# Optimization experiments

Hardware: AMD Instinct MI355X
Metric: run time of the kernel (lower is better)

Reference implementation:

```python
import math
import jax, jax.numpy as jnp
import numpy as np

B, S, HIDDEN = 1, 4096, 2048
HEADS, KVH = 16, 4
HD = HIDDEN // HEADS            # 128
GROUPS = HEADS // KVH           # 4
CHUNK = 1024                    # ring_attention_chunk_size
BASE = 500000.0
MAXPOS = 131072
ORIG = 8192
BFAST, BSLOW, MSCALE_CFG = 32.0, 1.0, 1.0
SCALING = MAXPOS / ORIG


def _yarn_inv_freq():
    dim = HD
    pos_freqs = BASE ** (np.arange(0, dim, 2, dtype=np.float32) / dim)
    extrap = 1.0 / pos_freqs
    interp = 1.0 / (SCALING * pos_freqs)
    low = max(math.floor(dim * math.log(ORIG / (BFAST * 2 * math.pi)) / (2 * math.log(BASE))), 0)
    high = min(math.ceil(dim * math.log(ORIG / (BSLOW * 2 * math.pi)) / (2 * math.log(BASE))), dim - 1)
    i = np.arange(dim // 2, dtype=np.float32)
    smooth = np.clip((i - low) / max(high - low, 1), 0.0, 1.0)  # i<low -> interp, i>high -> extrap
    inv = (1.0 - smooth) * interp + smooth * extrap
    return jnp.asarray(inv, jnp.float32)

INV_FREQ = _yarn_inv_freq()
MSCALE = (0.1 * math.log(SCALING) + 1.0) * MSCALE_CFG  # scaling > 1


def rotate_half(x):
    x1, x2 = jnp.split(x, 2, axis=-1)
    return jnp.concatenate((-x2, x1), axis=-1)


def ring_attention(q, k, v, chunk, causal=True):
    # q,k,v: [B,H,S,D]; kv_len divisible by chunk
    b, h, s, d = q.shape
    kv_len = k.shape[2]
    nc = kv_len // chunk
    scale = d ** (-0.5)
    k_chunks = jnp.moveaxis(k.reshape(b, h, nc, chunk, d), 2, 0)  # [nc,B,H,chunk,D]
    v_chunks = jnp.moveaxis(v.reshape(b, h, nc, chunk, d), 2, 0)
    kv_starts = jnp.arange(nc) * chunk
    q_idx = jnp.arange(s)[:, None]
    k_off = jnp.arange(chunk)[None, :]
    neg_inf = jnp.float32(-jnp.inf)

    def step(carry, inp):
        out, mx, se = carry
        kch, vch, kv_start = inp
        scores = jnp.einsum('bhqd,bhkd->bhqk', q, kch) * scale
        if causal:
            mask = (kv_start + k_off) > q_idx  # [S, chunk]
            scores = jnp.where(mask[None, None], neg_inf, scores)
        chunk_max = scores.max(axis=-1, keepdims=True)
        new_max = jnp.maximum(mx, chunk_max)
        exp_old = se * jnp.exp(mx - new_max)
        exp_chunk = jnp.exp(scores - new_max)
        exp_sum_chunk = exp_chunk.sum(axis=-1, keepdims=True)
        denom = exp_old + exp_sum_chunk + 1e-10
        out = out * (se / denom) + jnp.einsum('bhqk,bhkd->bhqd', exp_chunk, vch) / denom
        return (out, new_max, exp_old + exp_sum_chunk), None

    init = (jnp.zeros_like(q),
            jnp.full((b, h, s, 1), -jnp.inf, dtype=q.dtype),
            jnp.zeros((b, h, s, 1), dtype=q.dtype))
    (out, _, _), _ = jax.lax.scan(step, init, (k_chunks, v_chunks, kv_starts))
    return out


def setup_inputs() -> dict:
    key = jax.random.key(0)
    ks = jax.random.split(key, 5)
    hidden_states = jax.random.normal(ks[0], (B, S, HIDDEN), dtype=jnp.float32)
    position_ids = jnp.broadcast_to(jnp.arange(S, dtype=jnp.int32)[None, :], (B, S))
    sd = 1.0 / math.sqrt(HIDDEN)
    Wq = jax.random.normal(ks[1], (HIDDEN, HEADS * HD), dtype=jnp.float32) * sd
    Wk = jax.random.normal(ks[2], (HIDDEN, KVH * HD), dtype=jnp.float32) * sd
    Wv = jax.random.normal(ks[3], (HIDDEN, KVH * HD), dtype=jnp.float32) * sd
    Wo = jax.random.normal(ks[4], (HEADS * HD, HIDDEN), dtype=jnp.float32) * sd
    return {'hidden_states': hidden_states, 'position_ids': position_ids,
            'Wq': Wq, 'Wk': Wk, 'Wv': Wv, 'Wo': Wo}


def reference(hidden_states, position_ids, Wq, Wk, Wv, Wo):
    b, s, _ = hidden_states.shape
    q = (hidden_states @ Wq).reshape(b, s, HEADS, HD).transpose(0, 2, 1, 3)
    k = (hidden_states @ Wk).reshape(b, s, KVH, HD).transpose(0, 2, 1, 3)
    v = (hidden_states @ Wv).reshape(b, s, KVH, HD).transpose(0, 2, 1, 3)
    # YaRN rope
    freqs = position_ids.astype(jnp.float32)[:, :, None] * INV_FREQ[None, None, :]  # [B,S,HD/2]
    emb = jnp.concatenate((freqs, freqs), axis=-1)  # [B,S,HD]
    cos = (jnp.cos(emb) * MSCALE)[:, None]  # [B,1,S,HD]
    sin = (jnp.sin(emb) * MSCALE)[:, None]
    q = q * cos + rotate_half(q) * sin
    k = k * cos + rotate_half(k) * sin
    # GQA expand
    k = jnp.repeat(k, GROUPS, axis=1)
    v = jnp.repeat(v, GROUPS, axis=1)
    # ring path: use_ring_attention and kv_len > chunk
    attn = ring_attention(q, k, v, CHUNK, causal=True)
    attn = attn.transpose(0, 2, 1, 3).reshape(b, s, HEADS * HD)
    return attn @ Wo
```

## Files before the change

kernel.cpp:

```cpp
#include <hip/hip_runtime.h>
#include <cstdint>
#include <cstddef>


typedef unsigned short u16;
typedef unsigned int u32;
typedef float f32x4 __attribute__((ext_vector_type(4)));
typedef __bf16 bf16x8 __attribute__((ext_vector_type(8)));

__device__ __forceinline__ u16 f2bf(float f) {
    union { float f; u32 u; } v; v.f = f;
    u32 u = v.u;
    u += 0x7fffu + ((u >> 16) & 1u);
    return (u16)(u >> 16);
}
__device__ __forceinline__ float bf2f(u16 b) {
    union { u32 u; float f; } v; v.u = ((u32)b) << 16;
    return v.f;
}
__device__ __forceinline__ u16 f2h(float f) {
    union { _Float16 h; u16 u; } v; v.h = (_Float16)f; return v.u;
}
__device__ __forceinline__ float h2f(u16 u) {
    union { u16 u; _Float16 h; } v; v.u = u; return (float)v.h;
}

__device__ __forceinline__ void load16_to_lds(const void* g, void* l) {
    __builtin_amdgcn_global_load_lds((const __attribute__((address_space(1))) u32*)g,
                                     (__attribute__((address_space(3))) u32*)l,
                                     16, 0, 0);
}

#define MFMA16(a, b, c) __builtin_amdgcn_mfma_f32_16x16x32_bf16((a), (b), (c), 0, 0, 0)

__global__ __launch_bounds__(256) void convert_f32_bf16(const float* __restrict__ X,
                                                        u16* __restrict__ Y) {
    const int base = (blockIdx.x * 1024 + threadIdx.x) * 4;
#pragma unroll
    for (int k = 0; k < 4; ++k) {
        const int i = base + k * 1024;
        const float4 v = *(const float4*)(X + i);
        union { u16 s[4]; uint2 u; } pk;
        pk.s[0] = f2bf(v.x); pk.s[1] = f2bf(v.y); pk.s[2] = f2bf(v.z); pk.s[3] = f2bf(v.w);
        *(uint2*)(Y + i) = pk.u;
    }
}

__global__ __launch_bounds__(256) void transpose_w4(const float* __restrict__ Wq,
                                                    const float* __restrict__ Wk,
                                                    const float* __restrict__ Wv,
                                                    const float* __restrict__ Wo,
                                                    u16* __restrict__ Wt,
                                                    u16* __restrict__ Wot) {
    __shared__ float tile[64][65];
    const int bx = blockIdx.x;
    const float* W; u16* dst; int N, n0;
    if (bx < 32)      { W = Wq; dst = Wt;                          N = 2048; n0 = bx * 64; }
    else if (bx < 40) { W = Wk; dst = Wt + (size_t)2048 * 2048;    N = 512;  n0 = (bx - 32) * 64; }
    else if (bx < 48) { W = Wv; dst = Wt + (size_t)2560 * 2048;    N = 512;  n0 = (bx - 40) * 64; }
    else              { W = Wo; dst = Wot;                         N = 2048; n0 = (bx - 48) * 64; }
    const int k0 = blockIdx.y * 64;
    const int tc = threadIdx.x & 63, tr = threadIdx.x >> 6;
#pragma unroll
    for (int i = 0; i < 64; i += 4)
        tile[tc][tr + i] = W[(size_t)(k0 + tr + i) * N + n0 + tc];
    __syncthreads();
#pragma unroll
    for (int i = 0; i < 64; i += 4)
        dst[(size_t)(n0 + tr + i) * 2048 + k0 + tc] = f2bf(tile[tr + i][tc]);
}

__device__ __forceinline__ void store_out(float* p, float v) { *p = v; }
__device__ __forceinline__ void store_out(u16* p, float v) { *p = f2bf(v); }

template <typename OutT>
__global__ __launch_bounds__(256) void gemm_bt(const u16* __restrict__ A,
                                               const u16* __restrict__ Bt,
                                               OutT* __restrict__ C,
                                               int M, int N, int K) {
    __shared__ __align__(16) u16 sA[8192];
    __shared__ __align__(16) u16 sB[8192];
    const int t = threadIdx.x;
    const int lane = t & 63, w = t >> 6;
    const int quad = lane >> 4, l15 = lane & 15;
    const int m0 = blockIdx.x << 7, n0 = blockIdx.y << 7;
    const int wr4 = (w >> 1) * 4, wc4 = (w & 1) * 4;
    f32x4 acc[4][4] = {};
    for (int k0 = 0; k0 < K; k0 += 64) {
        __syncthreads();
#pragma unroll
        for (int r = 0; r < 2; ++r) {
            const int f = w * 2 + r;
#pragma unroll
            for (int kc = 0; kc < 2; ++kc) {
                load16_to_lds(A + (size_t)(m0 + f * 16 + l15) * K + k0 + kc * 32 + quad * 8,
                              sA + (f * 2 + kc) * 512);
                load16_to_lds(Bt + (size_t)(n0 + f * 16 + l15) * K + k0 + kc * 32 + quad * 8,
                              sB + (f * 2 + kc) * 512);
            }
        }
        __syncthreads();
#pragma unroll
        for (int kc = 0; kc < 2; ++kc) {
            bf16x8 af[4], bb[4];
#pragma unroll
            for (int i = 0; i < 4; ++i)
                af[i] = *(const bf16x8*)(sA + ((wr4 + i) * 2 + kc) * 512 + lane * 8);
#pragma unroll
            for (int j = 0; j < 4; ++j)
                bb[j] = *(const bf16x8*)(sB + ((wc4 + j) * 2 + kc) * 512 + lane * 8);
#pragma unroll
            for (int i = 0; i < 4; ++i)
#pragma unroll
                for (int j = 0; j < 4; ++j)
                    acc[i][j] = MFMA16(af[i], bb[j], acc[i][j]);
        }
    }
#pragma unroll
    for (int i = 0; i < 4; ++i)
#pragma unroll
        for (int j = 0; j < 4; ++j) {
            const int row = m0 + (w >> 1) * 64 + i * 16 + quad * 4;
            const int col = n0 + (w & 1) * 64 + j * 16 + l15;
#pragma unroll
            for (int r = 0; r < 4; ++r)
                store_out(C + (size_t)(row + r) * N + col, acc[i][j][r]);
        }
}

__global__ __launch_bounds__(256) void rope_vt_kernel(u16* __restrict__ QKV,
                                                      u16* __restrict__ Vt,
                                                      const int* __restrict__ pos_ids) {
    __shared__ u16 tile[64 * 72];
    if (blockIdx.x >= 20480) {
        const int b = blockIdx.x - 20480;
        const int k0 = (b & 63) * 64, d0 = ((b >> 6) & 1) * 64, kvh = b >> 7;
        const int t = threadIdx.x;
#pragma unroll
        for (int k = 0; k < 4; ++k) {
            const int u = t + k * 256;
            const int key = u >> 4, dg = u & 15;
            const uint2 v = *(const uint2*)(QKV + (size_t)(k0 + key) * 3072 + 2560 + kvh * 128 + d0 + dg * 4);
            *(uint2*)(tile + key * 72 + dg * 4) = v;
        }
        __syncthreads();
#pragma unroll
        for (int k = 0; k < 4; ++k) {
            const int u = t + k * 256;
            const int d = u >> 4, kg = u & 15;
            union { u16 s[4]; uint2 v; } pk;
#pragma unroll
            for (int i = 0; i < 4; ++i) pk.s[i] = tile[(kg * 4 + i) * 72 + d];
            *(uint2*)(Vt + (size_t)(kvh * 128 + d0 + d) * 4096 + k0 + kg * 4) = pk.v;
        }
        return;
    }
    const int idx = blockIdx.x * 256 + threadIdx.x;
    const int NQ = 4096 * 16 * 64;
    u16* p;
    int s, i;
    if (idx < NQ) {
        s = idx >> 10;
        const int hi = idx & 1023;
        const int h = hi >> 6;
        i = hi & 63;
        p = QKV + (size_t)s * 3072 + h * 128 + i;
    } else {
        const int k = idx - NQ;
        s = k >> 8;
        const int hi = k & 255;
        const int h = hi >> 6;
        i = hi & 63;
        p = QKV + (size_t)s * 3072 + 2048 + h * 128 + i;
    }
    const float pf = (float)pos_ids[s];
    const float fi = (float)i;
    const float pos_freq = powf(500000.0f, fi * (1.0f / 64.0f));
    const float inv_ex = 1.0f / pos_freq;
    const float inv_in = inv_ex * (1.0f / 16.0f);
    const float sm = fminf(fmaxf((fi - 18.0f) * (1.0f / 17.0f), 0.0f), 1.0f);
    const float inv = (1.0f - sm) * inv_in + sm * inv_ex;
    const float ph = pf * inv;
    const float MS = 1.2772588722239781f;
    const float cs = cosf(ph) * MS, sn = sinf(ph) * MS;
    const float x1 = bf2f(p[0]), x2 = bf2f(p[64]);
    p[0] = f2bf(x1 * cs - x2 * sn);
    p[64] = f2bf(x2 * cs + x1 * sn);
}

__device__ __forceinline__ void stage_kv(const u16* __restrict__ QKV,
                                         const u16* __restrict__ Vt,
                                         int kt0, int kvh, int w, int l15, int quad,
                                         u16* bK, u16* bV) {
    const u16* gk = QKV + (size_t)(kt0 + w * 16 + l15) * 3072 + 2048 + kvh * 128 + quad * 8;
#pragma unroll
    for (int kc = 0; kc < 4; ++kc)
        load16_to_lds(gk + kc * 32, bK + (w * 4 + kc) * 512);
#pragma unroll
    for (int r = 0; r < 4; ++r) {
        const int dt = w * 2 + (r >> 1), ks = r & 1;
        load16_to_lds(Vt + (size_t)(kvh * 128 + dt * 16 + l15) * 4096 + kt0 + ks * 32 + quad * 8,
                      bV + (dt * 2 + ks) * 512);
    }
}

__global__ __launch_bounds__(256, 2) void attn_partial(const u16* __restrict__ QKV,
                                                       const u16* __restrict__ Vt,
                                                       u16* __restrict__ part,
                                                       float* __restrict__ ml) {
    __shared__ __align__(16) u16 sK[8192];
    __shared__ __align__(16) u16 sV[8192];
    __shared__ __align__(16) u16 sP[8192];

    const int t = threadIdx.x;
    const int lane = t & 63, w = t >> 6;
    const int quad = lane >> 4, l15 = lane & 15;
    const int bid = blockIdx.x;
    const int u = bid >> 4, h = bid & 15, kvh = h >> 2;

    int qb, c;
    if (u < 8)       { qb = 8 + u; c = 0; }
    else if (u < 24) { const int r = u - 8;  qb = 16 + (r >> 1); c = r & 1; }
    else if (u < 48) { const int r = u - 24; const int q3 = r / 3; qb = 24 + q3; c = r - q3 * 3; }
    else             { const int r = u - 48; const int k = r >> 2; const int g0 = r & 3;
                       qb = g0 * 8 + (7 - k); c = g0; }
    const int g = qb >> 3;
    const int q0 = qb << 7, kv0 = c << 10;
    const int jmax = (c == g) ? (2 * (qb & 7) + 2) : 16;

    {
        u16* dst0 = (w < 2) ? sK : sV;
        const int fbase = (w & 1) * 8;
#pragma unroll
        for (int idx = 0; idx < 8; ++idx) {
            const int qg = idx >> 2, kc = idx & 3;
            load16_to_lds(QKV + (size_t)(q0 + w * 32 + qg * 16 + l15) * 3072 + h * 128 + kc * 32 + quad * 8,
                          dst0 + (fbase + idx) * 512);
        }
    }
    __syncthreads();
    bf16x8 af[2][4];
    {
        const u16* src0 = (w < 2) ? sK : sV;
        const int fbase = (w & 1) * 8;
#pragma unroll
        for (int qg = 0; qg < 2; ++qg)
#pragma unroll
            for (int kc = 0; kc < 4; ++kc)
                af[qg][kc] = *(const bf16x8*)(src0 + (fbase + qg * 4 + kc) * 512 + lane * 8);
    }

    float m_c[2] = {-1e30f, -1e30f}, l_c[2] = {0.0f, 0.0f};
    f32x4 o_c[8][2] = {};
    const float SCALE = 0.08838834764831845f;

    for (int j = 0; j < jmax; ++j) {
        const int kt0 = kv0 + (j << 6);
        __syncthreads();
        stage_kv(QKV, Vt, kt0, kvh, w, l15, quad, sK, sV);
        __syncthreads();

        f32x4 sacc[4][2] = {};
#pragma unroll
        for (int j4 = 0; j4 < 4; ++j4)
#pragma unroll
            for (int kc = 0; kc < 4; ++kc) {
                const bf16x8 kf = *(const bf16x8*)(sK + (j4 * 4 + kc) * 512 + lane * 8);
                sacc[j4][0] = MFMA16(kf, af[0][kc], sacc[j4][0]);
                sacc[j4][1] = MFMA16(kf, af[1][kc], sacc[j4][1]);
            }

        const bool diag = (c == g) && ((j >> 1) == (qb & 7));
        if (diag) {
#pragma unroll
            for (int j4 = 0; j4 < 4; ++j4)
#pragma unroll
                for (int qg = 0; qg < 2; ++qg) {
                    const int qrow = q0 + w * 32 + qg * 16 + l15;
#pragma unroll
                    for (int r = 0; r < 4; ++r) {
                        const int key = kt0 + j4 * 16 + quad * 4 + r;
                        sacc[j4][qg][r] = (key > qrow) ? -1e30f : sacc[j4][qg][r] * SCALE;
                    }
                }
        } else {
#pragma unroll
            for (int j4 = 0; j4 < 4; ++j4)
#pragma unroll
                for (int qg = 0; qg < 2; ++qg)
#pragma unroll
                    for (int r = 0; r < 4; ++r)
                        sacc[j4][qg][r] *= SCALE;
        }

#pragma unroll
        for (int qg = 0; qg < 2; ++qg) {
            float mx = -1e30f;
#pragma unroll
            for (int j4 = 0; j4 < 4; ++j4)
#pragma unroll
                for (int r = 0; r < 4; ++r) mx = fmaxf(mx, sacc[j4][qg][r]);
            mx = fmaxf(mx, __shfl_xor(mx, 16, 64));
            mx = fmaxf(mx, __shfl_xor(mx, 32, 64));
            const float mn = fmaxf(m_c[qg], mx);
            const float alpha = __expf(m_c[qg] - mn);
            float ps = 0.0f;
#pragma unroll
            for (int j4 = 0; j4 < 4; ++j4)
#pragma unroll
                for (int r = 0; r < 4; ++r) {
                    const float pe = __expf(sacc[j4][qg][r] - mn);
                    sacc[j4][qg][r] = pe;
                    ps += pe;
                }
            ps += __shfl_xor(ps, 16, 64);
            ps += __shfl_xor(ps, 32, 64);
            l_c[qg] = l_c[qg] * alpha + ps;
            m_c[qg] = mn;
#pragma unroll
            for (int dt = 0; dt < 8; ++dt) o_c[dt][qg] *= alpha;
        }

#pragma unroll
        for (int ks = 0; ks < 2; ++ks)
#pragma unroll
            for (int jj = 0; jj < 2; ++jj) {
                const int j4 = ks * 2 + jj;
                const int quadp = jj * 2 + (quad >> 1);
#pragma unroll
                for (int qg = 0; qg < 2; ++qg)
#pragma unroll
                    for (int pr = 0; pr < 2; ++pr) {
                        const int r = pr * 2;
                        const int jje = (quad & 1) * 4 + r;
                        const u32 pk = ((u32)f2bf(sacc[j4][qg][r + 1]) << 16) | f2bf(sacc[j4][qg][r]);
                        *(u32*)(sP + w * 2048 + (qg * 2 + ks) * 512 + (quadp * 16 + l15) * 8 + jje) = pk;
                    }
            }

#pragma unroll
        for (int ks = 0; ks < 2; ++ks) {
            const bf16x8 pf0 = *(const bf16x8*)(sP + w * 2048 + (0 * 2 + ks) * 512 + lane * 8);
            const bf16x8 pf1 = *(const bf16x8*)(sP + w * 2048 + (1 * 2 + ks) * 512 + lane * 8);
#pragma unroll
            for (int dt = 0; dt < 8; ++dt) {
                const bf16x8 vf = *(const bf16x8*)(sV + (dt * 2 + ks) * 512 + lane * 8);
                o_c[dt][0] = MFMA16(vf, pf0, o_c[dt][0]);
                o_c[dt][1] = MFMA16(vf, pf1, o_c[dt][1]);
            }
        }
    }

#pragma unroll
    for (int qg = 0; qg < 2; ++qg) {
        const float invl = 1.0f / l_c[qg];
        const int q = w * 32 + qg * 16 + l15;
#pragma unroll
        for (int dt = 0; dt < 8; ++dt)
#pragma unroll
            for (int r = 0; r < 4; ++r)
                part[(size_t)bid * 16384 + (dt * 16 + quad * 4 + r) * 128 + q] =
                    f2h(o_c[dt][qg][r] * invl);
        if (quad == 0) {
            ml[(size_t)bid * 256 + q * 2] = m_c[qg];
            ml[(size_t)bid * 256 + q * 2 + 1] = l_c[qg];
        }
    }
}

__global__ __launch_bounds__(256) void attn_merge(const u16* __restrict__ part,
                                                  const float* __restrict__ ml,
                                                  u16* __restrict__ attn) {
    const int b = blockIdx.x;
    const int qb = b >> 4, h = b & 15;
    const int g = qb >> 3;
    const int t = threadIdx.x;
    const int qrow = t & 127;
    const int d0 = blockIdx.y * 64 + (t >> 7) * 32;

    float o[32];
#pragma unroll
    for (int i = 0; i < 32; ++i) o[i] = 0.0f;
    float m_g = -1e30f, l_g = 0.0f;

    for (int c = 0; c <= g; ++c) {
        int u;
        if (c == g)      u = 48 + (7 - (qb & 7)) * 4 + g;
        else if (g == 1) u = qb - 8;
        else if (g == 2) u = 8 + (qb - 16) * 2 + c;
        else             u = 24 + (qb - 24) * 3 + c;
        const int tile = u * 16 + h;
        const float m_c = ml[(size_t)tile * 256 + qrow * 2];
        const float l_c = ml[(size_t)tile * 256 + qrow * 2 + 1];
        const float mn = fmaxf(m_g, m_c);
        const float a = l_g * __expf(m_g - mn);
        const float eC = __expf(m_c - mn);
        const float sE = l_c * eC;
        const float d = a + sE + 1e-10f;
        const float f_old = l_g / d;
        const float f_new = sE / d;
#pragma unroll
        for (int i = 0; i < 32; ++i) {
            const float v = h2f(part[(size_t)tile * 16384 + (d0 + i) * 128 + qrow]);
            o[i] = o[i] * f_old + v * f_new;
        }
        l_g = a + sE;
        m_g = mn;
    }

    u16* dst = attn + (size_t)(qb * 128 + qrow) * 2048 + h * 128 + d0;
#pragma unroll
    for (int kq = 0; kq < 4; ++kq) {
        union { u16 s[8]; uint4 v; } pk;
#pragma unroll
        for (int i = 0; i < 8; ++i) pk.s[i] = f2bf(o[kq * 8 + i]);
        *(uint4*)(dst + kq * 8) = pk.v;
    }
}

extern "C" void kernel_launch(void* const* d_in, const int* in_sizes, int n_in,
                              void* d_out, int out_size, void* d_ws, size_t ws_size,
                              hipStream_t stream) {
    const float* X  = (const float*)d_in[0];
    const int* pos  = (const int*)d_in[1];
    const float* Wq = (const float*)d_in[2];
    const float* Wk = (const float*)d_in[3];
    const float* Wv = (const float*)d_in[4];
    const float* Wo = (const float*)d_in[5];
    float* out = (float*)d_out;
    char* ws = (char*)d_ws;

    u16*   part = (u16*)(ws);
    u16*   Xbf  = (u16*)(ws);
    u16*   Wt   = (u16*)(ws + 16777216);
    u16*   QKV  = (u16*)(ws + 41943040);
    u16*   attn = (u16*)(ws + 41943040);
    u16*   Vt   = (u16*)(ws + 67108864);
    float* ml   = (float*)(ws + 71303168);
    u16*   Wot  = (u16*)(ws + 72613888);

    convert_f32_bf16<<<2048, 256, 0, stream>>>(X, Xbf);
    transpose_w4<<<dim3(80, 32), 256, 0, stream>>>(Wq, Wk, Wv, Wo, Wt, Wot);

    gemm_bt<u16><<<dim3(32, 24), 256, 0, stream>>>(Xbf, Wt, QKV, 4096, 3072, 2048);

    rope_vt_kernel<<<20992, 256, 0, stream>>>(QKV, Vt, pos);

    attn_partial<<<1280, 256, 0, stream>>>(QKV, Vt, part, ml);
    attn_merge<<<dim3(512, 2), 256, 0, stream>>>(part, ml, attn);

    gemm_bt<float><<<dim3(32, 16), 256, 0, stream>>>(attn, Wot, out, 4096, 2048, 2048);
}
```

Measured before the change: 448.2 us.

## Shuffle softmax probabilities in registers, drop LDS P buffer, use hardware exp2

The attention partial kernel no longer stages the bf16 probability tile through shared memory. It repacks P into MFMA operand layout with cross-lane shuffles, which frees 16 KB of LDS and lets the launch bound ask for 4 blocks per SM instead of 2. The scale multiply is folded into a single fma feeding a raw v_exp_f32 (exp2). The max and sum reductions are also restructured as trees. The shuffles add ALU and cross-lane traffic, and the higher occupancy target may force register spills given the large o_c accumulator.

Result: slower. 607.4 us (+35.5%).

```diff
diff --git a/kernel.cpp b/kernel.cpp
--- a/kernel.cpp
+++ b/kernel.cpp
@@ -23,6 +23,16 @@
 }
 __device__ __forceinline__ float h2f(u16 u) {
     union { u16 u; _Float16 h; } v; v.u = u; return (float)v.h;
+}
+__device__ __forceinline__ u32 pkbf(float lo, float hi) {
+    union { __bf16 h[2]; u32 u; } v;
+    v.h[0] = (__bf16)lo; v.h[1] = (__bf16)hi;
+    return v.u;
+}
+__device__ __forceinline__ float exp2_hw(float x) {
+    float r;
+    asm("v_exp_f32 %0, %1" : "=v"(r) : "v"(x));
+    return r;
 }
 
 __device__ __forceinline__ void load16_to_lds(const void* g, void* l) {
@@ -204,13 +214,12 @@
     }
 }
 
-__global__ __launch_bounds__(256, 2) void attn_partial(const u16* __restrict__ QKV,
+__global__ __launch_bounds__(256, 4) void attn_partial(const u16* __restrict__ QKV,
                                                        const u16* __restrict__ Vt,
                                                        u16* __restrict__ part,
                                                        float* __restrict__ ml) {
     __shared__ __align__(16) u16 sK[8192];
     __shared__ __align__(16) u16 sV[8192];
-    __shared__ __align__(16) u16 sP[8192];
 
     const int t = threadIdx.x;
     const int lane = t & 63, w = t >> 6;
@@ -253,6 +262,12 @@
     float m_c[2] = {-1e30f, -1e30f}, l_c[2] = {0.0f, 0.0f};
     f32x4 o_c[8][2] = {};
     const float SCALE = 0.08838834764831845f;
+    const float LOG2E = 1.4426950408889634f;
+    const float CS = SCALE * LOG2E;
+
+    const int srcLo = ((quad & 1) << 5) | l15;
+    const int srcHi = srcLo | 16;
+    const bool selB = (quad & 2) != 0;
 
     for (int j = 0; j < jmax; ++j) {
         const int kt0 = kv0 + (j << 6);
@@ -280,73 +295,75 @@
 #pragma unroll
                     for (int r = 0; r < 4; ++r) {
                         const int key = kt0 + j4 * 16 + quad * 4 + r;
-                        sacc[j4][qg][r] = (key > qrow) ? -1e30f : sacc[j4][qg][r] * SCALE;
+                        if (key > qrow) sacc[j4][qg][r] = -1e30f;
                     }
                 }
-        } else {
-#pragma unroll
-            for (int j4 = 0; j4 < 4; ++j4)
-#pragma unroll
-                for (int qg = 0; qg < 2; ++qg)
-#pragma unroll
-                    for (int r = 0; r < 4; ++r)
-                        sacc[j4][qg][r] *= SCALE;
-        }
-
+        }
+
+        bf16x8 pf[2][2];
 #pragma unroll
         for (int qg = 0; qg < 2; ++qg) {
-            float mx = -1e30f;
-#pragma unroll
-            for (int j4 = 0; j4 < 4; ++j4)
-#pragma unroll
-                for (int r = 0; r < 4; ++r) mx = fmaxf(mx, sacc[j4][qg][r]);
+            f32x4 v01, v23;
+#pragma unroll
+            for (int r = 0; r < 4; ++r) {
+                v01[r] = fmaxf(sacc[0][qg][r], sacc[1][qg][r]);
+                v23[r] = fmaxf(sacc[2][qg][r], sacc[3][qg][r]);
+            }
+            float mx = fmaxf(fmaxf(fmaxf(v01[0], v01[1]), fmaxf(v01[2], v01[3])),
+                             fmaxf(fmaxf(v23[0], v23[1]), fmaxf(v23[2], v23[3])));
             mx = fmaxf(mx, __shfl_xor(mx, 16, 64));
             mx = fmaxf(mx, __shfl_xor(mx, 32, 64));
-            const float mn = fmaxf(m_c[qg], mx);
-            const float alpha = __expf(m_c[qg] - mn);
-            float ps = 0.0f;
+            const float mn = fmaxf(m_c[qg], mx * SCALE);
+            const float alpha = exp2_hw((m_c[qg] - mn) * LOG2E);
+            const float kk = -mn * LOG2E;
 #pragma unroll
             for (int j4 = 0; j4 < 4; ++j4)
 #pragma unroll
-                for (int r = 0; r < 4; ++r) {
-                    const float pe = __expf(sacc[j4][qg][r] - mn);
-                    sacc[j4][qg][r] = pe;
-                    ps += pe;
-                }
+                for (int r = 0; r < 4; ++r)
+                    sacc[j4][qg][r] = exp2_hw(fmaf(sacc[j4][qg][r], CS, kk));
+            const f32x4 pv = (sacc[0][qg] + sacc[1][qg]) + (sacc[2][qg] + sacc[3][qg]);
+            float ps = (pv[0] + pv[1]) + (pv[2] + pv[3]);
             ps += __shfl_xor(ps, 16, 64);
             ps += __shfl_xor(ps, 32, 64);
             l_c[qg] = l_c[qg] * alpha + ps;
             m_c[qg] = mn;
 #pragma unroll
             for (int dt = 0; dt < 8; ++dt) o_c[dt][qg] *= alpha;
-        }
-
-#pragma unroll
-        for (int ks = 0; ks < 2; ++ks)
-#pragma unroll
-            for (int jj = 0; jj < 2; ++jj) {
-                const int j4 = ks * 2 + jj;
-                const int quadp = jj * 2 + (quad >> 1);
-#pragma unroll
-                for (int qg = 0; qg < 2; ++qg)
-#pragma unroll
-                    for (int pr = 0; pr < 2; ++pr) {
-                        const int r = pr * 2;
-                        const int jje = (quad & 1) * 4 + r;
-                        const u32 pk = ((u32)f2bf(sacc[j4][qg][r + 1]) << 16) | f2bf(sacc[j4][qg][r]);
-                        *(u32*)(sP + w * 2048 + (qg * 2 + ks) * 512 + (quadp * 16 + l15) * 8 + jje) = pk;
-                    }
-            }
+
+            u32 pk[4][2];
+#pragma unroll
+            for (int j4 = 0; j4 < 4; ++j4) {
+                pk[j4][0] = pkbf(sacc[j4][qg][0], sacc[j4][qg][1]);
+                pk[j4][1] = pkbf(sacc[j4][qg][2], sacc[j4][qg][3]);
+            }
+#pragma unroll
+            for (int ks = 0; ks < 2; ++ks) {
+                union { u32 wd[4]; bf16x8 v; } bu;
+                const u32 a0 = pk[2 * ks][0], a1 = pk[2 * ks][1];
+                const u32 b0 = pk[2 * ks + 1][0], b1 = pk[2 * ks + 1][1];
+                const u32 xa0 = (u32)__shfl((int)a0, srcLo, 64);
+                const u32 xb0 = (u32)__shfl((int)b0, srcLo, 64);
+                bu.wd[0] = selB ? xb0 : xa0;
+                const u32 xa1 = (u32)__shfl((int)a1, srcLo, 64);
+                const u32 xb1 = (u32)__shfl((int)b1, srcLo, 64);
+                bu.wd[1] = selB ? xb1 : xa1;
+                const u32 ya0 = (u32)__shfl((int)a0, srcHi, 64);
+                const u32 yb0 = (u32)__shfl((int)b0, srcHi, 64);
+                bu.wd[2] = selB ? yb0 : ya0;
+                const u32 ya1 = (u32)__shfl((int)a1, srcHi, 64);
+                const u32 yb1 = (u32)__shfl((int)b1, srcHi, 64);
+                bu.wd[3] = selB ? yb1 : ya1;
+                pf[qg][ks] = bu.v;
+            }
+        }
 
 #pragma unroll
         for (int ks = 0; ks < 2; ++ks) {
-            const bf16x8 pf0 = *(const bf16x8*)(sP + w * 2048 + (0 * 2 + ks) * 512 + lane * 8);
-            const bf16x8 pf1 = *(const bf16x8*)(sP + w * 2048 + (1 * 2 + ks) * 512 + lane * 8);
 #pragma unroll
             for (int dt = 0; dt < 8; ++dt) {
                 const bf16x8 vf = *(const bf16x8*)(sV + (dt * 2 + ks) * 512 + lane * 8);
-                o_c[dt][0] = MFMA16(vf, pf0, o_c[dt][0]);
-                o_c[dt][1] = MFMA16(vf, pf1, o_c[dt][1]);
+                o_c[dt][0] = MFMA16(vf, pf[0][ks], o_c[dt][0]);
+                o_c[dt][1] = MFMA16(vf, pf[1][ks], o_c[dt][1]);
             }
         }
     }
```
